# Performance work log

Hardware: AMD Instinct MI355X
Metric: run time of the kernel (lower is better)

## Reference

```python
import math
import jax, jax.numpy as jnp
import numpy as np

FACTOR = 5  # must match init_kwargs factor


def setup_inputs() -> dict:
    key = jax.random.key(0)
    B, L, H, D = 4, 2048, 16, 64
    k1, k2, k3, k4 = jax.random.split(key, 4)
    q = jax.random.normal(k1, (B, L, H, D), jnp.float32)
    k = jax.random.normal(k2, (B, L, H, D), jnp.float32)
    v = jax.random.normal(k3, (B, L, H, D), jnp.float32)
    sample_k = min(FACTOR * int(np.ceil(np.log(L))), L)  # = 40
    sample_idx = jax.random.randint(k4, (L, sample_k), 0, L)
    return {"q": q, "k": k, "v": v, "sample_idx": sample_idx, "attn_mask": 0}


def reference(q, k, v, sample_idx, attn_mask):
    B, L_q, H, D = q.shape
    L_k = k.shape[1]
    qh = jnp.swapaxes(q, 1, 2)  # [B,H,L_q,D]
    kh = jnp.swapaxes(k, 1, 2)  # [B,H,L_k,D]
    vh = jnp.swapaxes(v, 1, 2)  # [B,H,L_k,D]

    u_top = min(FACTOR * int(np.ceil(np.log(L_q))), L_q)

    # --- _prob_qk: sampled QK scores and sparsity measure M ---
    # k_s[b,h,q,s,d] = kh[b,h,sample_idx[q,s],d]  (per-query random key sample)
    k_s = kh[:, :, sample_idx, :]                       # [B,H,L_q,S,D]
    qk_sample = jnp.einsum('bhqd,bhqsd->bhqs', qh, k_s)  # [B,H,L_q,S]
    M = qk_sample.max(axis=-1) - qk_sample.sum(axis=-1) / L_k  # [B,H,L_q]
    _, M_top = jax.lax.top_k(M, u_top)                   # [B,H,u]

    # gather the top-u queries
    q_red = jnp.take_along_axis(qh, M_top[..., None], axis=2)  # [B,H,u,D]

    # dense scores of selected queries against all keys
    scores = jnp.einsum('bhud,bhkd->bhuk', q_red, kh) / math.sqrt(D)
    attn = jax.nn.softmax(scores, axis=-1)                     # [B,H,u,L_k]
    ctx = jnp.einsum('bhuk,bhkd->bhud', attn, vh)              # [B,H,u,D]

    # scatter context back into v at the selected query rows (RHS uses original v,
    # matching torch fancy-index assignment semantics)
    b_idx = jnp.arange(B)[:, None, None]
    h_idx = jnp.arange(H)[None, :, None]
    out = vh.at[b_idx, h_idx, M_top].set(ctx)
    return jnp.swapaxes(out, 1, 2)  # [B,L,H,D]
```

## Files before the change

### kernel.cpp

```cpp
#include <hip/hip_runtime.h>
#include <hip/hip_bf16.h>
#include <float.h>
#include <math.h>

constexpr int B = 4;
constexpr int L = 2048;
constexpr int H = 16;
constexpr int D = 64;
constexpr int U = 40;
constexpr int KROWS = 128;
constexpr int NRCH = 16;
constexpr int LPB = 16;
constexpr int CPB2 = 2048;

typedef float floatx4 __attribute__((ext_vector_type(4)));

template<int SKC>
__global__ __launch_bounds__(256) void compute_M_kernel2(const float* __restrict__ q,
                                                         const float* __restrict__ k,
                                                         const int* __restrict__ sidx,
                                                         float* __restrict__ M) {
    int blk = blockIdx.x;
    int xcd = blk & 7;
    int rest = blk >> 3;
    int bh_hi = rest & 7;
    int chunk = rest >> 3;
    int bh = bh_hi * 8 + xcd;
    int b = bh >> 4, h = bh & 15;

    int t = threadIdx.x;
    int lg = t >> 4;
    int dg = t & 15;

    __shared__ int s_idx[LPB * SKC];
    for (int i = t; i < LPB * SKC; i += 256)
        s_idx[i] = sidx[(size_t)(chunk * LPB) * SKC + i];
    __syncthreads();

    int l = chunk * LPB + lg;
    floatx4 qv = __builtin_nontemporal_load(
        reinterpret_cast<const floatx4*>(q + ((size_t)(b * L + l) * H + h) * D + dg * 4));

    float mx = -FLT_MAX;
    float sm = 0.f;
    #pragma unroll 4
    for (int s = 0; s < SKC; ++s) {
        int kidx = s_idx[lg * SKC + s];
        floatx4 kv = *reinterpret_cast<const floatx4*>(
            k + ((size_t)(b * L + kidx) * H + h) * D + dg * 4);
        float p = qv.x * kv.x + qv.y * kv.y + qv.z * kv.z + qv.w * kv.w;
        #pragma unroll
        for (int off = 8; off >= 1; off >>= 1) p += __shfl_xor(p, off, 16);
        mx = fmaxf(mx, p);
        sm += p;
    }
    if (dg == 0) {
        M[(size_t)bh * L + l] = mx - sm * (1.0f / (float)L);
    }
}

__global__ __launch_bounds__(256) void compute_M_kernel(const float* __restrict__ q,
                                                        const float* __restrict__ k,
                                                        const int* __restrict__ sidx,
                                                        float* __restrict__ M, int SK) {
    int bl = blockIdx.x;
    int b = bl / L;
    int l = bl % L;
    int t = threadIdx.x;
    int h = t >> 4;
    int dg = t & 15;

    const float* qrow = q + ((size_t)(b * L + l)) * H * D + h * D + dg * 4;
    float4 qv = *reinterpret_cast<const float4*>(qrow);

    float mx = -FLT_MAX;
    float sm = 0.f;
    for (int s = 0; s < SK; ++s) {
        int kidx = sidx[l * SK + s];
        const float* krow = k + ((size_t)(b * L + kidx)) * H * D + h * D + dg * 4;
        float4 kv = *reinterpret_cast<const float4*>(krow);
        float p = qv.x * kv.x + qv.y * kv.y + qv.z * kv.z + qv.w * kv.w;
        #pragma unroll
        for (int off = 8; off >= 1; off >>= 1) p += __shfl_xor(p, off, 16);
        mx = fmaxf(mx, p);
        sm += p;
    }
    if (dg == 0) {
        M[((size_t)(b * H + h)) * L + l] = mx - sm * (1.0f / (float)L);
    }
}

__global__ __launch_bounds__(256) void topk_copy_kernel(const float* __restrict__ M,
                                                        int* __restrict__ Mtop,
                                                        const float* __restrict__ v,
                                                        float* __restrict__ out, int n4) {
    int blk = blockIdx.x;
    int t = threadIdx.x;

    if (blk >= B * H) {
        int i = (blk - B * H) * 256 + t;
        int stride = CPB2 * 256;
        const floatx4* src = reinterpret_cast<const floatx4*>(v);
        floatx4* dst = reinterpret_cast<floatx4*>(out);
        for (; i < n4; i += stride) {
            floatx4 x = __builtin_nontemporal_load(src + i);
            __builtin_nontemporal_store(x, dst + i);
        }
        return;
    }
    if (t >= 64) return;

    int bh = blk;
    int lane = t;
    const float* m = M + (size_t)bh * L;

    float v_[32];
    #pragma unroll
    for (int j = 0; j < 32; ++j) v_[j] = m[j * 64 + lane];

    for (int u = 0; u < U; ++u) {
        float bv = -FLT_MAX;
        int bi = 0x7fffffff;
        #pragma unroll
        for (int j = 0; j < 32; ++j) {
            int idx = j * 64 + lane;
            bool take = (v_[j] > bv) || (v_[j] == bv && idx < bi);
            bv = take ? v_[j] : bv;
            bi = take ? idx : bi;
        }
        #pragma unroll
        for (int off = 1; off < 64; off <<= 1) {
            float ov = __shfl_xor(bv, off);
            int   oi = __shfl_xor(bi, off);
            bool take = (ov > bv) || (ov == bv && oi < bi);
            bv = take ? ov : bv;
            bi = take ? oi : bi;
        }
        if (lane == 0) Mtop[bh * U + u] = bi;
        #pragma unroll
        for (int j = 0; j < 32; ++j) {
            if (bi == j * 64 + lane) v_[j] = -FLT_MAX;
        }
    }
}

__global__ __launch_bounds__(256) void flash3_kernel(
        const float* __restrict__ q, const float* __restrict__ k,
        const float* __restrict__ v, const int* __restrict__ Mtop,
        float* __restrict__ pl, float* __restrict__ pacc) {
    int blk = blockIdx.x;
    int xcd = blk & 7;
    int bh = ((blk >> 3) & 7) * 8 + xcd;
    int rch = blk >> 6;
    int b = bh >> 4, h = bh & 15;
    int t = threadIdx.x;

    __shared__ __align__(16) float qs[U][D];
    __shared__ __align__(16) float lk[KROWS * D];
    __shared__ __align__(16) float pe[U][KROWS];
    __shared__ float redl[8][5];

    for (int i = t; i < U * D; i += 256) {
        int u = i >> 6, dd = i & 63;
        int qi = Mtop[bh * U + u];
        qs[u][dd] = q[((size_t)(b * L + qi) * H + h) * D + dd];
    }
    {
        const floatx4* ksrc = reinterpret_cast<const floatx4*>(
            k + ((size_t)(b * L + rch * KROWS) * H + h) * D);
        floatx4* ldst = reinterpret_cast<floatx4*>(lk);
        #pragma unroll
        for (int it = 0; it < (KROWS * 16) / 256; ++it) {
            int i = it * 256 + t;
            int row = i >> 4, c = i & 15;
            ldst[i] = ksrc[(size_t)row * (H * D / 4) + c];
        }
    }
    __syncthreads();

    int rg = t & 31;
    int ug = t >> 5;
    const floatx4* lk4 = reinterpret_cast<const floatx4*>(lk);

    float s0[5], s1[5], s2[5], s3[5];
    #pragma unroll
    for (int uu = 0; uu < 5; ++uu) { s0[uu] = 0.f; s1[uu] = 0.f; s2[uu] = 0.f; s3[uu] = 0.f; }

    #pragma unroll 4
    for (int jj = 0; jj < 16; ++jj) {
        int c = (jj + rg) & 15;
        floatx4 k0 = lk4[(rg * 4 + 0) * 16 + c];
        floatx4 k1 = lk4[(rg * 4 + 1) * 16 + c];
        floatx4 k2 = lk4[(rg * 4 + 2) * 16 + c];
        floatx4 k3 = lk4[(rg * 4 + 3) * 16 + c];
        #pragma unroll
        for (int uu = 0; uu < 5; ++uu) {
            floatx4 qj = *reinterpret_cast<const floatx4*>(&qs[ug * 5 + uu][c * 4]);
            s0[uu] = fmaf(k0.x, qj.x, fmaf(k0.y, qj.y, fmaf(k0.z, qj.z, fmaf(k0.w, qj.w, s0[uu]))));
            s1[uu] = fmaf(k1.x, qj.x, fmaf(k1.y, qj.y, fmaf(k1.z, qj.z, fmaf(k1.w, qj.w, s1[uu]))));
            s2[uu] = fmaf(k2.x, qj.x, fmaf(k2.y, qj.y, fmaf(k2.z, qj.z, fmaf(k2.w, qj.w, s2[uu]))));
            s3[uu] = fmaf(k3.x, qj.x, fmaf(k3.y, qj.y, fmaf(k3.z, qj.z, fmaf(k3.w, qj.w, s3[uu]))));
        }
    }

    #pragma unroll
    for (int uu = 0; uu < 5; ++uu) {
        int u = ug * 5 + uu;
        float e0 = __expf(s0[uu] * 0.125f);
        float e1 = __expf(s1[uu] * 0.125f);
        float e2 = __expf(s2[uu] * 0.125f);
        float e3 = __expf(s3[uu] * 0.125f);
        pe[u][rg * 4 + 0] = e0;
        pe[u][rg * 4 + 1] = e1;
        pe[u][rg * 4 + 2] = e2;
        pe[u][rg * 4 + 3] = e3;
        float sv = (e0 + e1) + (e2 + e3);
        #pragma unroll
        for (int off = 1; off <= 16; off <<= 1) sv += __shfl_xor(sv, off);
        if ((t & 31) == 0) redl[ug][uu] = sv;
    }
    __syncthreads();

    int d2 = t & 31;
    int ug2 = t >> 5;
    int d = d2 * 2;
    const float* vb = v + ((size_t)(b * L + rch * KROWS) * H + h) * D + d;
    float ax[5], ay[5];
    #pragma unroll
    for (int uu = 0; uu < 5; ++uu) { ax[uu] = 0.f; ay[uu] = 0.f; }
    #pragma unroll 2
    for (int row = 0; row < KROWS; row += 4) {
        float2 v0 = *reinterpret_cast<const float2*>(vb + (size_t)(row + 0) * (H * D));
        float2 v1 = *reinterpret_cast<const float2*>(vb + (size_t)(row + 1) * (H * D));
        float2 v2 = *reinterpret_cast<const float2*>(vb + (size_t)(row + 2) * (H * D));
        float2 v3 = *reinterpret_cast<const float2*>(vb + (size_t)(row + 3) * (H * D));
        #pragma unroll
        for (int uu = 0; uu < 5; ++uu) {
            float4 p4 = *reinterpret_cast<const float4*>(&pe[ug2 * 5 + uu][row]);
            ax[uu] = fmaf(p4.x, v0.x, fmaf(p4.y, v1.x, fmaf(p4.z, v2.x, fmaf(p4.w, v3.x, ax[uu]))));
            ay[uu] = fmaf(p4.x, v0.y, fmaf(p4.y, v1.y, fmaf(p4.z, v2.y, fmaf(p4.w, v3.y, ay[uu]))));
        }
    }

    size_t pb0 = (size_t)bh * U;
    #pragma unroll
    for (int uu = 0; uu < 5; ++uu) {
        int u = ug2 * 5 + uu;
        float2 o; o.x = ax[uu]; o.y = ay[uu];
        *reinterpret_cast<float2*>(&pacc[((pb0 + u) * NRCH + rch) * 64 + d]) = o;
    }
    if (t < U) {
        pl[(pb0 + t) * NRCH + rch] = redl[t / 5][t % 5];
    }
}

__global__ __launch_bounds__(256) void flash_merge_kernel(
        const float* __restrict__ pl, const float* __restrict__ pacc,
        const int* __restrict__ Mtop, float* __restrict__ out) {
    int idx = blockIdx.x * 256 + threadIdx.x;
    int dd = idx & 63;
    int bhu = idx >> 6;
    int bh = bhu / U;
    int b = bh / H, h = bh % H;

    float Lsum = 0.f;
    #pragma unroll
    for (int c = 0; c < NRCH; ++c) Lsum += pl[bhu * NRCH + c];

    float acc = 0.f;
    #pragma unroll
    for (int c = 0; c < NRCH; ++c)
        acc += pacc[((size_t)bhu * NRCH + c) * 64 + dd];

    int qi = Mtop[bhu];
    out[((size_t)(b * L + qi) * H + h) * D + dd] = acc / Lsum;
}

__global__ __launch_bounds__(256) void attn_kernel_fallback(
        const float* __restrict__ q, const float* __restrict__ k,
        const float* __restrict__ v, const int* __restrict__ Mtop,
        float* __restrict__ out) {
    int blk = blockIdx.x;
    int bh = blk / U;
    int u = blk % U;
    int b = bh / H;
    int h = bh % H;
    int qi = Mtop[bh * U + u];

    __shared__ float sc[L];
    __shared__ float qsf[D];
    __shared__ float red[4];
    __shared__ float ctx_s[4][D];

    int t = threadIdx.x;
    if (t < D) qsf[t] = q[((size_t)(b * L + qi)) * H * D + h * D + t];
    __syncthreads();

    float lm = -FLT_MAX;
    for (int i = t; i < L; i += 256) {
        const float* krow = k + ((size_t)(b * L + i)) * H * D + h * D;
        float acc = 0.f;
        #pragma unroll
        for (int dd = 0; dd < D; ++dd) acc += qsf[dd] * krow[dd];
        acc *= 0.125f;
        sc[i] = acc;
        lm = fmaxf(lm, acc);
    }
    #pragma unroll
    for (int off = 32; off >= 1; off >>= 1) lm = fmaxf(lm, __shfl_xor(lm, off));
    if ((t & 63) == 0) red[t >> 6] = lm;
    __syncthreads();
    float gm = fmaxf(fmaxf(red[0], red[1]), fmaxf(red[2], red[3]));

    float ls = 0.f;
    for (int i = t; i < L; i += 256) {
        float e = expf(sc[i] - gm);
        sc[i] = e;
        ls += e;
    }
    #pragma unroll
    for (int off = 32; off >= 1; off >>= 1) ls += __shfl_xor(ls, off);
    __syncthreads();
    if ((t & 63) == 0) red[t >> 6] = ls;
    __syncthreads();
    float inv = 1.0f / (red[0] + red[1] + red[2] + red[3]);

    int d = t & 63;
    int g = t >> 6;
    float acc = 0.f;
    for (int i = g; i < L; i += 4) {
        acc += sc[i] * v[((size_t)(b * L + i)) * H * D + h * D + d];
    }
    ctx_s[g][d] = acc;
    __syncthreads();
    if (g == 0) {
        float c = (ctx_s[0][d] + ctx_s[1][d] + ctx_s[2][d] + ctx_s[3][d]) * inv;
        out[((size_t)(b * L + qi)) * H * D + h * D + d] = c;
    }
}

extern "C" void kernel_launch(void* const* d_in, const int* in_sizes, int n_in,
                              void* d_out, int out_size, void* d_ws, size_t ws_size,
                              hipStream_t stream) {
    const float* q = (const float*)d_in[0];
    const float* k = (const float*)d_in[1];
    const float* v = (const float*)d_in[2];
    const int* sidx = (const int*)d_in[3];
    float* out = (float*)d_out;

    int SK = in_sizes[3] / L;

    size_t offM = 0;
    size_t offMtop = offM + (size_t)B * H * L * sizeof(float);
    size_t offPl = (offMtop + (size_t)B * H * U * sizeof(int) + 255) & ~(size_t)255;
    size_t offPacc = (offPl + (size_t)B * H * U * NRCH * sizeof(float) + 255) & ~(size_t)255;
    size_t needFlash = offPacc + (size_t)B * H * U * NRCH * 64 * sizeof(float);

    float* M = (float*)((char*)d_ws + offM);
    int* Mtop = (int*)((char*)d_ws + offMtop);
    float* pl = (float*)((char*)d_ws + offPl);
    float* pacc = (float*)((char*)d_ws + offPacc);

    int n4 = (B * L * H * D) / 4;

    if (SK == 40) {
        compute_M_kernel2<40><<<B * H * (L / LPB), 256, 0, stream>>>(q, k, sidx, M);
    } else {
        compute_M_kernel<<<B * L, 256, 0, stream>>>(q, k, sidx, M, SK);
    }

    topk_copy_kernel<<<B * H + CPB2, 256, 0, stream>>>(M, Mtop, v, out, n4);

    if (ws_size >= needFlash) {
        flash3_kernel<<<B * H * NRCH, 256, 0, stream>>>(q, k, v, Mtop, pl, pacc);
        flash_merge_kernel<<<B * H * U * 64 / 256, 256, 0, stream>>>(pl, pacc, Mtop, out);
    } else {
        attn_kernel_fallback<<<B * H * U, 256, 0, stream>>>(q, k, v, Mtop, out);
    }
}
```

Baseline: 197.7 us.

## Restructure sampled-QK kernel: 8-lane dot products, 8 samples per wave in parallel

The sparsity-measure kernel is remapped so each wave handles four queries, two at a time. Each query's dot product is split across 8 lanes with 8 floats per lane, and 8 sampled keys are processed concurrently per wave. This replaces the serial 40-iteration loop that ran a 16-lane shuffle reduction per sample, which should raise memory-level parallelism for the gathered key loads and cut shuffle count. The cost is an extra cross-group reduction of max and sum at the end, plus more registers per thread.

```diff
diff --git a/kernel.cpp b/kernel.cpp
--- a/kernel.cpp
+++ b/kernel.cpp
@@ -15,8 +15,13 @@
 
 typedef float floatx4 __attribute__((ext_vector_type(4)));
 
+__device__ inline float dot8(floatx4 a0, floatx4 a1, floatx4 b0, floatx4 b1) {
+    return a0.x * b0.x + a0.y * b0.y + a0.z * b0.z + a0.w * b0.w
+         + a1.x * b1.x + a1.y * b1.y + a1.z * b1.z + a1.w * b1.w;
+}
+
 template<int SKC>
-__global__ __launch_bounds__(256) void compute_M_kernel2(const float* __restrict__ q,
+__global__ __launch_bounds__(256) void compute_M_kernel4(const float* __restrict__ q,
                                                          const float* __restrict__ k,
                                                          const int* __restrict__ sidx,
                                                          float* __restrict__ M) {
@@ -27,35 +32,66 @@
     int chunk = rest >> 3;
     int bh = bh_hi * 8 + xcd;
     int b = bh >> 4, h = bh & 15;
-
     int t = threadIdx.x;
-    int lg = t >> 4;
-    int dg = t & 15;
 
     __shared__ int s_idx[LPB * SKC];
     for (int i = t; i < LPB * SKC; i += 256)
-        s_idx[i] = sidx[(size_t)(chunk * LPB) * SKC + i];
-    __syncthreads();
-
-    int l = chunk * LPB + lg;
-    floatx4 qv = __builtin_nontemporal_load(
-        reinterpret_cast<const floatx4*>(q + ((size_t)(b * L + l) * H + h) * D + dg * 4));
-
-    float mx = -FLT_MAX;
-    float sm = 0.f;
-    #pragma unroll 4
-    for (int s = 0; s < SKC; ++s) {
-        int kidx = s_idx[lg * SKC + s];
-        floatx4 kv = *reinterpret_cast<const floatx4*>(
-            k + ((size_t)(b * L + kidx) * H + h) * D + dg * 4);
-        float p = qv.x * kv.x + qv.y * kv.y + qv.z * kv.z + qv.w * kv.w;
-        #pragma unroll
-        for (int off = 8; off >= 1; off >>= 1) p += __shfl_xor(p, off, 16);
-        mx = fmaxf(mx, p);
-        sm += p;
-    }
-    if (dg == 0) {
-        M[(size_t)bh * L + l] = mx - sm * (1.0f / (float)L);
+        s_idx[i] = sidx[(size_t)chunk * LPB * SKC + i];
+    __syncthreads();
+
+    int w = t >> 6;
+    int lane = t & 63;
+    int g8 = lane >> 3;
+    int dpart = lane & 7;
+
+    #pragma unroll
+    for (int li = 0; li < 4; li += 2) {
+        int lga = w * 4 + li;
+        int lgb = lga + 1;
+        int la = chunk * LPB + lga;
+        int lb = la + 1;
+
+        const float* qra = q + ((size_t)(b * L + la) * H + h) * D;
+        const float* qrb = q + ((size_t)(b * L + lb) * H + h) * D;
+        floatx4 qa0 = *reinterpret_cast<const floatx4*>(qra + dpart * 4);
+        floatx4 qa1 = *reinterpret_cast<const floatx4*>(qra + 32 + dpart * 4);
+        floatx4 qb0 = *reinterpret_cast<const floatx4*>(qrb + dpart * 4);
+        floatx4 qb1 = *reinterpret_cast<const floatx4*>(qrb + 32 + dpart * 4);
+
+        int sa[SKC / 8], sb[SKC / 8];
+        #pragma unroll
+        for (int i = 0; i < SKC / 8; ++i) {
+            sa[i] = s_idx[lga * SKC + i * 8 + g8];
+            sb[i] = s_idx[lgb * SKC + i * 8 + g8];
+        }
+
+        float mxa = -FLT_MAX, sma = 0.f;
+        float mxb = -FLT_MAX, smb = 0.f;
+        #pragma unroll
+        for (int i = 0; i < SKC / 8; ++i) {
+            const float* kra = k + ((size_t)(b * L + sa[i]) * H + h) * D;
+            const float* krb = k + ((size_t)(b * L + sb[i]) * H + h) * D;
+            floatx4 ka0 = *reinterpret_cast<const floatx4*>(kra + dpart * 4);
+            floatx4 ka1 = *reinterpret_cast<const floatx4*>(kra + 32 + dpart * 4);
+            floatx4 kb0 = *reinterpret_cast<const floatx4*>(krb + dpart * 4);
+            floatx4 kb1 = *reinterpret_cast<const floatx4*>(krb + 32 + dpart * 4);
+            float pa = dot8(qa0, qa1, ka0, ka1);
+            float pb = dot8(qb0, qb1, kb0, kb1);
+            pa += __shfl_xor(pa, 1);  pb += __shfl_xor(pb, 1);
+            pa += __shfl_xor(pa, 2);  pb += __shfl_xor(pb, 2);
+            pa += __shfl_xor(pa, 4);  pb += __shfl_xor(pb, 4);
+            mxa = fmaxf(mxa, pa); sma += pa;
+            mxb = fmaxf(mxb, pb); smb += pb;
+        }
+        #pragma unroll
+        for (int off = 8; off <= 32; off <<= 1) {
+            mxa = fmaxf(mxa, __shfl_xor(mxa, off)); sma += __shfl_xor(sma, off);
+            mxb = fmaxf(mxb, __shfl_xor(mxb, off)); smb += __shfl_xor(smb, off);
+        }
+        if (lane == 0) {
+            M[(size_t)bh * L + la] = mxa - sma * (1.0f / (float)L);
+            M[(size_t)bh * L + lb] = mxb - smb * (1.0f / (float)L);
+        }
     }
 }
 
@@ -364,7 +400,7 @@
     int n4 = (B * L * H * D) / 4;
 
     if (SK == 40) {
-        compute_M_kernel2<40><<<B * H * (L / LPB), 256, 0, stream>>>(q, k, sidx, M);
+        compute_M_kernel4<40><<<B * H * (L / LPB), 256, 0, stream>>>(q, k, sidx, M);
     } else {
         compute_M_kernel<<<B * L, 256, 0, stream>>>(q, k, sidx, M, SK);
     }
```

New measurement: 194.2 us. About the same (-1.8%).
